# Performance work log

Hardware: AMD Instinct MI355X
Metric: run time of the kernel (lower is better)

The kernel has to match this reference:

```python
import jax, jax.numpy as jnp
import numpy as np

NUM_AA, EMB_DIM = 20, 16
H1, H2 = 128, 128
K, EXCLUDE = 64, 3
R_ON, R_CUT = 10.0, 12.0
RBF_CENTERS = (5.0, 6.0, 7.0, 8.0, 9.0, 10.0, 11.0)
RBF_WIDTH = 0.5
M = len(RBF_CENTERS)


def setup_inputs() -> dict:
    key = jax.random.key(0)
    ks = jax.random.split(key, 10)
    B, L = 8, 2048
    R = jax.random.normal(ks[0], (B, L, 3), dtype=jnp.float32) * 10.0  # spread distances over RBF range
    seq = jax.random.randint(ks[1], (B, L), 0, NUM_AA)
    emb_table = jax.random.normal(ks[2], (NUM_AA, EMB_DIM), dtype=jnp.float32) * 0.1
    in_dim = 3 * EMB_DIM
    W1 = jax.random.normal(ks[3], (in_dim, H1), dtype=jnp.float32) / np.sqrt(in_dim)
    b1 = jnp.zeros((H1,), jnp.float32)
    W2 = jax.random.normal(ks[4], (H1, H2), dtype=jnp.float32) / np.sqrt(H1)
    b2 = jnp.zeros((H2,), jnp.float32)
    W3 = jax.random.normal(ks[5], (H2, M), dtype=jnp.float32) / np.sqrt(H2)
    b3 = jnp.zeros((M,), jnp.float32)
    centers = jnp.asarray(RBF_CENTERS, jnp.float32)
    widths = jnp.full((M,), RBF_WIDTH, jnp.float32)
    return {"R": R, "seq": seq, "emb_table": emb_table,
            "W1": W1, "b1": b1, "W2": W2, "b2": b2, "W3": W3, "b3": b3,
            "centers": centers, "widths": widths}


def topk_nonbonded_pairs(R, K, exclude):
    # R: (B, L, 3) -> r: (B, L, K) distances, j: (B, L, K) neighbor indices
    B, L, _ = R.shape
    diff = R[:, :, None, :] - R[:, None, :, :]            # (B, L, L, 3)
    D = jnp.sqrt(jnp.sum(diff * diff, axis=-1) + 1e-12)   # (B, L, L)
    idx = jnp.arange(L)
    bonded = jnp.abs(idx[:, None] - idx[None, :]) <= exclude  # excludes self too
    D = jnp.where(bonded[None], jnp.inf, D)
    neg, j = jax.lax.top_k(-D, K)                          # K smallest distances
    return -neg, j


def smooth_switch(r, r_on, r_cut):
    t = jnp.clip((r - r_on) / (r_cut - r_on), 0.0, 1.0)
    return 1.0 - t * t * (3.0 - 2.0 * t)  # smoothstep down: 1 below r_on, 0 above r_cut


def distance_features(r, centers, widths):
    d = r[..., None] - centers  # (B, L, K, M)
    return jnp.exp(-(d * d) / (2.0 * widths * widths))


def reference(R, seq, emb_table, W1, b1, W2, b2, W3, b3, centers, widths):
    e = emb_table[seq]                                     # (B, L, d)
    r, j = topk_nonbonded_pairs(R, K, EXCLUDE)             # (B, L, K)
    e_j = jnp.take_along_axis(e[:, :, None, :], j[..., None], axis=1)  # wrong axis semantics avoided below
    # gather neighbor embeddings: e_j[b, i, k] = e[b, j[b, i, k]]
    e_j = jnp.take_along_axis(e[:, None, :, :].repeat(1, axis=1), j[..., None], axis=2) if False else \
          jnp.take_along_axis(e[:, :, None, :].transpose(0, 2, 1, 3).repeat(1, axis=0), j[..., None], axis=2) if False else \
          jax.vmap(lambda eb, jb: eb[jb])(e, j)            # (B, L, K, d)
    e_i = jnp.broadcast_to(e[:, :, None, :], e_j.shape)
    pair_feat = jnp.concatenate([e_i, e_j, e_i * e_j], axis=-1)  # (B, L, K, 3d)
    h = jax.nn.relu(pair_feat @ W1 + b1)
    h = jax.nn.relu(h @ W2 + b2)
    w = jax.nn.softplus(h @ W3 + b3)                       # (B, L, K, M)
    phi = distance_features(r, centers, widths)            # (B, L, K, M)
    att = -jnp.sum(w * phi, axis=-1)                       # (B, L, K)
    sw = smooth_switch(r, R_ON, R_CUT)
    return jnp.sum(att * sw, axis=(1, 2))                  # (B,)
```

## Files before the change

kernel.cpp:

```cpp
#include <hip/hip_runtime.h>
#include <math.h>

#define LSEQ 2048
#define KNB 64
#define BATCH 8
#define MRBF 7
#define NTILES 8192
#define NBLOCKS 512
#define BSCALE (255.0f/144.0f)

typedef __attribute__((ext_vector_type(8))) short short8;
typedef __attribute__((ext_vector_type(4))) float floatx4;

__device__ __forceinline__ unsigned short f2bf(float f) {
    unsigned u = __float_as_uint(f);
    u += 0x7fffu + ((u >> 16) & 1u);
    return (unsigned short)(u >> 16);
}
__device__ __forceinline__ unsigned pkbf(float a, float b) {
    return __builtin_amdgcn_perm(__float_as_uint(b) + 0x8000u,
                                 __float_as_uint(a) + 0x8000u, 0x07060302u);
}

__global__ __launch_bounds__(256, 2) void fused_kernel(
    const float* __restrict__ R, const int* __restrict__ seq,
    const float* __restrict__ emb,
    const float* __restrict__ W1, const float* __restrict__ b1,
    const float* __restrict__ W2, const float* __restrict__ b2,
    const float* __restrict__ W3, const float* __restrict__ b3,
    const float* __restrict__ centers, const float* __restrict__ widths,
    float* __restrict__ out)
{
    __shared__ __align__(16) unsigned short lds[32768];
    unsigned short* H1s = lds;
    unsigned short* Xs  = lds + 16384;
    unsigned short* H2s = lds + 16384;
    int*      nbrL    = (int*)lds;
    unsigned* hist    = (unsigned*)((char*)lds + 512);
    float*    cand_d2 = (float*)((char*)lds + 2560);
    int*      cand_j  = (int*)((char*)lds + 3584);
    int*      tctr    = (int*)((char*)lds + 4608);
    int* sB    = tctr + 0;
    int* sNeed = tctr + 2;
    int* oPos  = tctr + 4;
    int* cCnt  = tctr + 6;
    int* fCnt  = tctr + 8;
    __shared__ float bacc[BATCH];

    const int tid  = threadIdx.x;
    const int lane = tid & 63;
    const int wv   = tid >> 6;
    const int l15  = lane & 15;
    const int q    = lane >> 4;

    short8 w1f[2][2], w2f[2][4], w3f[4];
    float b1v[2][4], b2v[2][4];
    #pragma unroll
    for (int mtl = 0; mtl < 2; mtl++) {
        int m = (2*wv + mtl)*16 + l15;
        #pragma unroll
        for (int d = 0; d < 4; d++) {
            b1v[mtl][d] = b1[(2*wv + mtl)*16 + q*4 + d];
            b2v[mtl][d] = b2[(2*wv + mtl)*16 + q*4 + d];
        }
        #pragma unroll
        for (int kt = 0; kt < 2; kt++)
            #pragma unroll
            for (int jj = 0; jj < 8; jj++) {
                int k = kt*32 + q*8 + jj;
                w1f[mtl][kt][jj] = (short)((k < 48) ? f2bf(W1[k*128 + m]) : 0);
            }
        #pragma unroll
        for (int kt = 0; kt < 4; kt++)
            #pragma unroll
            for (int jj = 0; jj < 8; jj++) {
                int k = kt*32 + q*8 + jj;
                w2f[mtl][kt][jj] = (short)f2bf(W2[k*128 + m]);
            }
    }
    #pragma unroll
    for (int kt = 0; kt < 4; kt++)
        #pragma unroll
        for (int jj = 0; jj < 8; jj++) {
            int k = kt*32 + q*8 + jj;
            w3f[kt][jj] = (short)((l15 < MRBF) ? f2bf(W3[k*MRBF + l15]) : 0);
        }
    float b3C[4], cen[4], i2w[4];
    #pragma unroll
    for (int d = 0; d < 4; d++) {
        int rb = q*4 + d;
        bool ok = rb < MRBF;
        b3C[d] = ok ? b3[rb] : 0.f;
        cen[d] = ok ? centers[rb] : 0.f;
        float wd = ok ? widths[rb] : 1.f;
        i2w[d] = 0.5f / (wd*wd);
    }
    if (tid < BATCH) bacc[tid] = 0.f;

    const int pl = tid >> 1, half = tid & 1;
    const int s7p = pl & 7;
    float rloc = 0.f;

    for (int tile = blockIdx.x; tile < NTILES; tile += NBLOCKS) {
        const int b     = tile >> 10;
        const int ibase = (tile & 1023) << 1;
        const float* Rb = R + ((b << 11) * 3);

        __syncthreads();

        hist[tid] = 0u; hist[tid + 256] = 0u;
        if (tid < 2) { oPos[tid] = 0; cCnt[tid] = 0; fCnt[tid] = 0; }

        float px[8], py[8], pz[8];
        {
            const float4* rp = (const float4*)(Rb + tid*24);
            float4 f0=rp[0], f1=rp[1], f2=rp[2], f3=rp[3], f4=rp[4], f5=rp[5];
            px[0]=f0.x; py[0]=f0.y; pz[0]=f0.z;
            px[1]=f0.w; py[1]=f1.x; pz[1]=f1.y;
            px[2]=f1.z; py[2]=f1.w; pz[2]=f2.x;
            px[3]=f2.y; py[3]=f2.z; pz[3]=f2.w;
            px[4]=f3.x; py[4]=f3.y; pz[4]=f3.z;
            px[5]=f3.w; py[5]=f4.x; pz[5]=f4.y;
            px[6]=f4.z; py[6]=f4.w; pz[6]=f5.x;
            px[7]=f5.y; py[7]=f5.z; pz[7]=f5.w;
        }
        float cx0 = Rb[3*ibase+0], cy0 = Rb[3*ibase+1], cz0 = Rb[3*ibase+2];
        float cx1 = Rb[3*ibase+3], cy1 = Rb[3*ibase+4], cz1 = Rb[3*ibase+5];
        __syncthreads();

        float d2r[2][8];
        #pragma unroll
        for (int u = 0; u < 8; u++) {
            int j = tid*8 + u;
            #pragma unroll
            for (int c = 0; c < 2; c++) {
                float dx = (c ? cx1 : cx0) - px[u];
                float dy = (c ? cy1 : cy0) - py[u];
                float dz = (c ? cz1 : cz0) - pz[u];
                float d2 = dx*dx + dy*dy + dz*dz;
                int dd = j - (ibase + c); dd = dd < 0 ? -dd : dd;
                if (dd <= 3) d2 = 1e30f;
                d2r[c][u] = d2;
                if (d2 < 144.0f)
                    atomicAdd(&hist[(c<<8) + (int)(d2*BSCALE)], 1u);
            }
        }
        __syncthreads();

        if (wv < 2) {
            unsigned h4[4]; unsigned s = 0;
            #pragma unroll
            for (int v = 0; v < 4; v++) { h4[v] = hist[(wv<<8) + lane*4 + v]; s += h4[v]; }
            unsigned inc = s;
            #pragma unroll
            for (int off = 1; off < 64; off <<= 1) {
                unsigned n = __shfl_up(inc, off, 64);
                if (lane >= off) inc += n;
            }
            unsigned tot = __shfl(inc, 63, 64);
            unsigned excl = inc - s;
            if (tot < 64u) {
                if (lane == 0) { sB[wv] = 255; sNeed[wv] = 64 - (int)tot; }
            } else if (excl < 64u && 64u <= inc) {
                unsigned cc = excl;
                #pragma unroll
                for (int v = 0; v < 4; v++) {
                    if (cc < 64u && 64u <= cc + h4[v]) { sB[wv] = lane*4+v; sNeed[wv] = 64 - (int)cc; }
                    cc += h4[v];
                }
            }
        }
        __syncthreads();

        #pragma unroll
        for (int u = 0; u < 8; u++) {
            int j = tid*8 + u;
            #pragma unroll
            for (int c = 0; c < 2; c++) {
                float d2 = d2r[c][u];
                int B = sB[c];
                if (d2 < 144.0f) {
                    int key = (int)(d2*BSCALE);
                    if (key < B) {
                        int pos = atomicAdd(&oPos[c], 1);
                        nbrL[(c<<6) + pos] = j;
                    } else if (key == B) {
                        int cc = atomicAdd(&cCnt[c], 1);
                        if (cc < 128) { cand_d2[(c<<7)+cc] = d2; cand_j[(c<<7)+cc] = j; }
                    }
                } else if (B == 255 && d2 < 1e29f) {
                    int t = atomicAdd(&fCnt[c], 1);
                    if (t < sNeed[c]) {
                        int pos = atomicAdd(&oPos[c], 1);
                        nbrL[(c<<6) + pos] = j;
                    }
                }
            }
        }
        __syncthreads();

        if (wv < 2) {
            int B = sB[wv];
            if (B != 255) {
                int cn = cCnt[wv]; if (cn > 128) cn = 128;
                int need = sNeed[wv];
                for (int ci = lane; ci < cn; ci += 64) {
                    float dv = cand_d2[(wv<<7)+ci]; int jv = cand_j[(wv<<7)+ci];
                    int rank = 0;
                    for (int x = 0; x < cn; x++) {
                        float dx2 = cand_d2[(wv<<7)+x]; int jx2 = cand_j[(wv<<7)+x];
                        rank += (dx2 < dv) || (dx2 == dv && jx2 < jv);
                    }
                    if (rank < need) {
                        int pos = atomicAdd(&oPos[wv], 1);
                        nbrL[(wv<<6) + pos] = jv;
                    }
                }
            }
        }
        __syncthreads();

        {
            int c  = pl >> 6;
            int bi = (b << 11) + ibase + c;
            int j  = nbrL[pl];
            int rowj = (b << 11) + j;
            int si = seq[bi], sj = seq[rowj];
            const float4* ei = (const float4*)(emb + si*16 + half*8);
            const float4* ej = (const float4*)(emb + sj*16 + half*8);
            float4 eA0 = ei[0], eA1 = ei[1], eB0 = ej[0], eB1 = ej[1];
            int rb = pl*64;
            uint4 vA = make_uint4(pkbf(eA0.x,eA0.y), pkbf(eA0.z,eA0.w),
                                  pkbf(eA1.x,eA1.y), pkbf(eA1.z,eA1.w));
            uint4 vB = make_uint4(pkbf(eB0.x,eB0.y), pkbf(eB0.z,eB0.w),
                                  pkbf(eB1.x,eB1.y), pkbf(eB1.z,eB1.w));
            uint4 vP = make_uint4(pkbf(eA0.x*eB0.x, eA0.y*eB0.y),
                                  pkbf(eA0.z*eB0.z, eA0.w*eB0.w),
                                  pkbf(eA1.x*eB1.x, eA1.y*eB1.y),
                                  pkbf(eA1.z*eB1.z, eA1.w*eB1.w));
            *(uint4*)&Xs[rb + (((0|half)^s7p)<<3)] = vA;
            *(uint4*)&Xs[rb + (((2|half)^s7p)<<3)] = vB;
            *(uint4*)&Xs[rb + (((4|half)^s7p)<<3)] = vP;
            *(uint4*)&Xs[rb + (((6|half)^s7p)<<3)] = make_uint4(0u,0u,0u,0u);
            if (!half) {
                float dx = R[bi*3+0]-R[rowj*3+0];
                float dy = R[bi*3+1]-R[rowj*3+1];
                float dz = R[bi*3+2]-R[rowj*3+2];
                rloc = sqrtf(dx*dx + dy*dy + dz*dz + 1e-12f);
            }
        }
        __syncthreads();

        #pragma unroll
        for (int nt = 0; nt < 8; nt++) {
            int row = nt*16 + l15;
            int s7 = l15 & 7;
            const unsigned short* xr = Xs + row*64;
            short8 x0 = *(const short8*)&xr[(( q    ^ s7) << 3)];
            short8 x1 = *(const short8*)&xr[(((4|q) ^ s7) << 3)];
            #pragma unroll
            for (int mtl = 0; mtl < 2; mtl++) {
                floatx4 acc = {b1v[mtl][0], b1v[mtl][1], b1v[mtl][2], b1v[mtl][3]};
                acc = __builtin_amdgcn_mfma_f32_16x16x32_bf16(w1f[mtl][0], x0, acc, 0, 0, 0);
                acc = __builtin_amdgcn_mfma_f32_16x16x32_bf16(w1f[mtl][1], x1, acc, 0, 0, 0);
                int chnk = (((2*wv + mtl)*2 + (q>>1)) ^ s7);
                *(uint2*)&H1s[row*128 + (chnk<<3) + ((q&1)<<2)] =
                    make_uint2(pkbf(fmaxf(acc[0],0.f), fmaxf(acc[1],0.f)),
                               pkbf(fmaxf(acc[2],0.f), fmaxf(acc[3],0.f)));
            }
        }
        __syncthreads();

        #pragma unroll
        for (int nt = 0; nt < 8; nt++) {
            int row = nt*16 + l15;
            int s7 = l15 & 7;
            const unsigned short* hr = H1s + row*128;
            short8 hf0 = *(const short8*)&hr[(( q     ^ s7) << 3)];
            short8 hf1 = *(const short8*)&hr[((( 4|q) ^ s7) << 3)];
            short8 hf2 = *(const short8*)&hr[((( 8|q) ^ s7) << 3)];
            short8 hf3 = *(const short8*)&hr[(((12|q) ^ s7) << 3)];
            #pragma unroll
            for (int mtl = 0; mtl < 2; mtl++) {
                floatx4 acc = {b2v[mtl][0], b2v[mtl][1], b2v[mtl][2], b2v[mtl][3]};
                acc = __builtin_amdgcn_mfma_f32_16x16x32_bf16(w2f[mtl][0], hf0, acc, 0, 0, 0);
                acc = __builtin_amdgcn_mfma_f32_16x16x32_bf16(w2f[mtl][1], hf1, acc, 0, 0, 0);
                acc = __builtin_amdgcn_mfma_f32_16x16x32_bf16(w2f[mtl][2], hf2, acc, 0, 0, 0);
                acc = __builtin_amdgcn_mfma_f32_16x16x32_bf16(w2f[mtl][3], hf3, acc, 0, 0, 0);
                int chnk = (((2*wv + mtl)*2 + (q>>1)) ^ s7);
                *(uint2*)&H2s[row*128 + (chnk<<3) + ((q&1)<<2)] =
                    make_uint2(pkbf(fmaxf(acc[0],0.f), fmaxf(acc[1],0.f)),
                               pkbf(fmaxf(acc[2],0.f), fmaxf(acc[3],0.f)));
            }
        }
        __syncthreads();

        float esum = 0.f;
        #pragma unroll
        for (int ntl = 0; ntl < 2; ntl++) {
            int nt = 2*wv + ntl;
            int row = nt*16 + l15;
            int s7 = l15 & 7;
            const unsigned short* hr = H2s + row*128;
            floatx4 a3 = {b3C[0], b3C[1], b3C[2], b3C[3]};
            #pragma unroll
            for (int kt = 0; kt < 4; kt++) {
                short8 hf = *(const short8*)&hr[((((kt<<2)|q) ^ s7) << 3)];
                a3 = __builtin_amdgcn_mfma_f32_16x16x32_bf16(w3f[kt], hf, a3, 0, 0, 0);
            }
            float rr = __shfl(rloc, (ntl<<5) + 2*l15, 64);
            if (rr < 12.0f) {
                float att = 0.f;
                #pragma unroll
                for (int d = 0; d < 4; d++) {
                    if (q*4 + d < MRBF) {
                        float x = a3[d];
                        float sp = fmaxf(x, 0.f) + __logf(1.f + __expf(-fabsf(x)));
                        float df = rr - cen[d];
                        att += sp * __expf(-df*df*i2w[d]);
                    }
                }
                att += __shfl_xor(att, 16, 64);
                att += __shfl_xor(att, 32, 64);
                float t = fminf(fmaxf((rr - 10.f)*0.5f, 0.f), 1.f);
                float sw = 1.f - t*t*(3.f - 2.f*t);
                esum -= att * sw;
            }
        }
        #pragma unroll
        for (int off = 1; off < 64; off <<= 1)
            esum += __shfl_xor(esum, off, 64);
        if (lane == 0) atomicAdd(&bacc[b], esum * 0.25f);
    }
    __syncthreads();
    if (tid < BATCH) atomicAdd(&out[tid], bacc[tid]);
}

extern "C" void kernel_launch(void* const* d_in, const int* in_sizes, int n_in,
                              void* d_out, int out_size, void* d_ws, size_t ws_size,
                              hipStream_t stream) {
    const float* R       = (const float*)d_in[0];
    const int*   seq     = (const int*)  d_in[1];
    const float* emb     = (const float*)d_in[2];
    const float* W1      = (const float*)d_in[3];
    const float* b1      = (const float*)d_in[4];
    const float* W2      = (const float*)d_in[5];
    const float* b2      = (const float*)d_in[6];
    const float* W3      = (const float*)d_in[7];
    const float* b3      = (const float*)d_in[8];
    const float* centers = (const float*)d_in[9];
    const float* widths  = (const float*)d_in[10];
    float* out = (float*)d_out;

    hipMemsetAsync(d_out, 0, out_size * sizeof(float), stream);

    fused_kernel<<<NBLOCKS, 256, 0, stream>>>(R, seq, emb, W1, b1, W2, b2, W3, b3,
                                              centers, widths, out);
}
```

Baseline: 253.7 us.

## Process four query rows per block iteration and shrink LDS for three blocks per CU

```diff
diff --git a/kernel.cpp b/kernel.cpp
--- a/kernel.cpp
+++ b/kernel.cpp
@@ -5,8 +5,8 @@
 #define KNB 64
 #define BATCH 8
 #define MRBF 7
-#define NTILES 8192
-#define NBLOCKS 512
+#define NGROUPS 4096
+#define NBLOCKS 768
 #define BSCALE (255.0f/144.0f)
 
 typedef __attribute__((ext_vector_type(8))) short short8;
@@ -22,7 +22,7 @@
                                  __float_as_uint(a) + 0x8000u, 0x07060302u);
 }
 
-__global__ __launch_bounds__(256, 2) void fused_kernel(
+__global__ __launch_bounds__(256, 3) void fused_kernel(
     const float* __restrict__ R, const int* __restrict__ seq,
     const float* __restrict__ emb,
     const float* __restrict__ W1, const float* __restrict__ b1,
@@ -31,20 +31,19 @@
     const float* __restrict__ centers, const float* __restrict__ widths,
     float* __restrict__ out)
 {
-    __shared__ __align__(16) unsigned short lds[32768];
-    unsigned short* H1s = lds;
-    unsigned short* Xs  = lds + 16384;
-    unsigned short* H2s = lds + 16384;
-    int*      nbrL    = (int*)lds;
-    unsigned* hist    = (unsigned*)((char*)lds + 512);
-    float*    cand_d2 = (float*)((char*)lds + 2560);
-    int*      cand_j  = (int*)((char*)lds + 3584);
-    int*      tctr    = (int*)((char*)lds + 4608);
+    __shared__ __align__(16) unsigned short lds[25088];
+    int* nbrL = (int*)lds;
+    unsigned short* Xs = lds + 512;
+    unsigned short* Hs = lds + 8704;
+    unsigned* hist    = (unsigned*)((char*)lds + 1024);
+    float*    cand_d2 = (float*)((char*)lds + 5120);
+    int*      cand_j  = (int*)((char*)lds + 7168);
+    int*      tctr    = (int*)((char*)lds + 9216);
     int* sB    = tctr + 0;
-    int* sNeed = tctr + 2;
-    int* oPos  = tctr + 4;
-    int* cCnt  = tctr + 6;
-    int* fCnt  = tctr + 8;
+    int* sNeed = tctr + 4;
+    int* oPos  = tctr + 8;
+    int* cCnt  = tctr + 12;
+    int* fCnt  = tctr + 16;
     __shared__ float bacc[BATCH];
 
     const int tid  = threadIdx.x;
@@ -101,15 +100,13 @@
     const int s7p = pl & 7;
     float rloc = 0.f;
 
-    for (int tile = blockIdx.x; tile < NTILES; tile += NBLOCKS) {
-        const int b     = tile >> 10;
-        const int ibase = (tile & 1023) << 1;
+    for (int grp = blockIdx.x; grp < NGROUPS; grp += NBLOCKS) {
+        const int b     = grp >> 9;
+        const int ibase = (grp & 511) << 2;
         const float* Rb = R + ((b << 11) * 3);
 
-        __syncthreads();
-
-        hist[tid] = 0u; hist[tid + 256] = 0u;
-        if (tid < 2) { oPos[tid] = 0; cCnt[tid] = 0; fCnt[tid] = 0; }
+        hist[tid] = 0u; hist[tid+256] = 0u; hist[tid+512] = 0u; hist[tid+768] = 0u;
+        if (tid < 4) { oPos[tid] = 0; cCnt[tid] = 0; fCnt[tid] = 0; }
 
         float px[8], py[8], pz[8];
         {
@@ -124,19 +121,22 @@
             px[6]=f4.z; py[6]=f4.w; pz[6]=f5.x;
             px[7]=f5.y; py[7]=f5.z; pz[7]=f5.w;
         }
-        float cx0 = Rb[3*ibase+0], cy0 = Rb[3*ibase+1], cz0 = Rb[3*ibase+2];
-        float cx1 = Rb[3*ibase+3], cy1 = Rb[3*ibase+4], cz1 = Rb[3*ibase+5];
-        __syncthreads();
-
-        float d2r[2][8];
+        float cx[4], cy[4], cz[4];
+        #pragma unroll
+        for (int c = 0; c < 4; c++) {
+            cx[c] = Rb[3*(ibase+c)+0];
+            cy[c] = Rb[3*(ibase+c)+1];
+            cz[c] = Rb[3*(ibase+c)+2];
+        }
+        __syncthreads();
+
+        float d2r[4][8];
         #pragma unroll
         for (int u = 0; u < 8; u++) {
             int j = tid*8 + u;
             #pragma unroll
-            for (int c = 0; c < 2; c++) {
-                float dx = (c ? cx1 : cx0) - px[u];
-                float dy = (c ? cy1 : cy0) - py[u];
-                float dz = (c ? cz1 : cz0) - pz[u];
+            for (int c = 0; c < 4; c++) {
+                float dx = cx[c]-px[u], dy = cy[c]-py[u], dz = cz[c]-pz[u];
                 float d2 = dx*dx + dy*dy + dz*dz;
                 int dd = j - (ibase + c); dd = dd < 0 ? -dd : dd;
                 if (dd <= 3) d2 = 1e30f;
@@ -147,7 +147,7 @@
         }
         __syncthreads();
 
-        if (wv < 2) {
+        {
             unsigned h4[4]; unsigned s = 0;
             #pragma unroll
             for (int v = 0; v < 4; v++) { h4[v] = hist[(wv<<8) + lane*4 + v]; s += h4[v]; }
@@ -176,7 +176,7 @@
         for (int u = 0; u < 8; u++) {
             int j = tid*8 + u;
             #pragma unroll
-            for (int c = 0; c < 2; c++) {
+            for (int c = 0; c < 4; c++) {
                 float d2 = d2r[c][u];
                 int B = sB[c];
                 if (d2 < 144.0f) {
@@ -199,7 +199,7 @@
         }
         __syncthreads();
 
-        if (wv < 2) {
+        {
             int B = sB[wv];
             if (B != 255) {
                 int cn = cCnt[wv]; if (cn > 128) cn = 128;
@@ -220,111 +220,124 @@
         }
         __syncthreads();
 
-        {
-            int c  = pl >> 6;
-            int bi = (b << 11) + ibase + c;
-            int j  = nbrL[pl];
-            int rowj = (b << 11) + j;
-            int si = seq[bi], sj = seq[rowj];
-            const float4* ei = (const float4*)(emb + si*16 + half*8);
-            const float4* ej = (const float4*)(emb + sj*16 + half*8);
-            float4 eA0 = ei[0], eA1 = ei[1], eB0 = ej[0], eB1 = ej[1];
-            int rb = pl*64;
-            uint4 vA = make_uint4(pkbf(eA0.x,eA0.y), pkbf(eA0.z,eA0.w),
-                                  pkbf(eA1.x,eA1.y), pkbf(eA1.z,eA1.w));
-            uint4 vB = make_uint4(pkbf(eB0.x,eB0.y), pkbf(eB0.z,eB0.w),
-                                  pkbf(eB1.x,eB1.y), pkbf(eB1.z,eB1.w));
-            uint4 vP = make_uint4(pkbf(eA0.x*eB0.x, eA0.y*eB0.y),
-                                  pkbf(eA0.z*eB0.z, eA0.w*eB0.w),
-                                  pkbf(eA1.x*eB1.x, eA1.y*eB1.y),
-                                  pkbf(eA1.z*eB1.z, eA1.w*eB1.w));
-            *(uint4*)&Xs[rb + (((0|half)^s7p)<<3)] = vA;
-            *(uint4*)&Xs[rb + (((2|half)^s7p)<<3)] = vB;
-            *(uint4*)&Xs[rb + (((4|half)^s7p)<<3)] = vP;
-            *(uint4*)&Xs[rb + (((6|half)^s7p)<<3)] = make_uint4(0u,0u,0u,0u);
-            if (!half) {
-                float dx = R[bi*3+0]-R[rowj*3+0];
-                float dy = R[bi*3+1]-R[rowj*3+1];
-                float dz = R[bi*3+2]-R[rowj*3+2];
-                rloc = sqrtf(dx*dx + dy*dy + dz*dz + 1e-12f);
-            }
-        }
-        __syncthreads();
-
-        #pragma unroll
-        for (int nt = 0; nt < 8; nt++) {
-            int row = nt*16 + l15;
-            int s7 = l15 & 7;
-            const unsigned short* xr = Xs + row*64;
-            short8 x0 = *(const short8*)&xr[(( q    ^ s7) << 3)];
-            short8 x1 = *(const short8*)&xr[(((4|q) ^ s7) << 3)];
-            #pragma unroll
-            for (int mtl = 0; mtl < 2; mtl++) {
-                floatx4 acc = {b1v[mtl][0], b1v[mtl][1], b1v[mtl][2], b1v[mtl][3]};
-                acc = __builtin_amdgcn_mfma_f32_16x16x32_bf16(w1f[mtl][0], x0, acc, 0, 0, 0);
-                acc = __builtin_amdgcn_mfma_f32_16x16x32_bf16(w1f[mtl][1], x1, acc, 0, 0, 0);
-                int chnk = (((2*wv + mtl)*2 + (q>>1)) ^ s7);
-                *(uint2*)&H1s[row*128 + (chnk<<3) + ((q&1)<<2)] =
-                    make_uint2(pkbf(fmaxf(acc[0],0.f), fmaxf(acc[1],0.f)),
-                               pkbf(fmaxf(acc[2],0.f), fmaxf(acc[3],0.f)));
-            }
-        }
-        __syncthreads();
-
-        #pragma unroll
-        for (int nt = 0; nt < 8; nt++) {
-            int row = nt*16 + l15;
-            int s7 = l15 & 7;
-            const unsigned short* hr = H1s + row*128;
-            short8 hf0 = *(const short8*)&hr[(( q     ^ s7) << 3)];
-            short8 hf1 = *(const short8*)&hr[((( 4|q) ^ s7) << 3)];
-            short8 hf2 = *(const short8*)&hr[((( 8|q) ^ s7) << 3)];
-            short8 hf3 = *(const short8*)&hr[(((12|q) ^ s7) << 3)];
-            #pragma unroll
-            for (int mtl = 0; mtl < 2; mtl++) {
-                floatx4 acc = {b2v[mtl][0], b2v[mtl][1], b2v[mtl][2], b2v[mtl][3]};
-                acc = __builtin_amdgcn_mfma_f32_16x16x32_bf16(w2f[mtl][0], hf0, acc, 0, 0, 0);
-                acc = __builtin_amdgcn_mfma_f32_16x16x32_bf16(w2f[mtl][1], hf1, acc, 0, 0, 0);
-                acc = __builtin_amdgcn_mfma_f32_16x16x32_bf16(w2f[mtl][2], hf2, acc, 0, 0, 0);
-                acc = __builtin_amdgcn_mfma_f32_16x16x32_bf16(w2f[mtl][3], hf3, acc, 0, 0, 0);
-                int chnk = (((2*wv + mtl)*2 + (q>>1)) ^ s7);
-                *(uint2*)&H2s[row*128 + (chnk<<3) + ((q&1)<<2)] =
-                    make_uint2(pkbf(fmaxf(acc[0],0.f), fmaxf(acc[1],0.f)),
-                               pkbf(fmaxf(acc[2],0.f), fmaxf(acc[3],0.f)));
-            }
-        }
-        __syncthreads();
-
         float esum = 0.f;
-        #pragma unroll
-        for (int ntl = 0; ntl < 2; ntl++) {
-            int nt = 2*wv + ntl;
-            int row = nt*16 + l15;
-            int s7 = l15 & 7;
-            const unsigned short* hr = H2s + row*128;
-            floatx4 a3 = {b3C[0], b3C[1], b3C[2], b3C[3]};
-            #pragma unroll
-            for (int kt = 0; kt < 4; kt++) {
-                short8 hf = *(const short8*)&hr[((((kt<<2)|q) ^ s7) << 3)];
-                a3 = __builtin_amdgcn_mfma_f32_16x16x32_bf16(w3f[kt], hf, a3, 0, 0, 0);
-            }
-            float rr = __shfl(rloc, (ntl<<5) + 2*l15, 64);
-            if (rr < 12.0f) {
-                float att = 0.f;
-                #pragma unroll
-                for (int d = 0; d < 4; d++) {
-                    if (q*4 + d < MRBF) {
-                        float x = a3[d];
-                        float sp = fmaxf(x, 0.f) + __logf(1.f + __expf(-fabsf(x)));
-                        float df = rr - cen[d];
-                        att += sp * __expf(-df*df*i2w[d]);
-                    }
-                }
-                att += __shfl_xor(att, 16, 64);
-                att += __shfl_xor(att, 32, 64);
-                float t = fminf(fmaxf((rr - 10.f)*0.5f, 0.f), 1.f);
-                float sw = 1.f - t*t*(3.f - 2.f*t);
-                esum -= att * sw;
+        #pragma unroll 1
+        for (int sub = 0; sub < 2; sub++) {
+            {
+                int c2 = (sub << 1) | (pl >> 6);
+                int bi = (b << 11) + ibase + c2;
+                int j  = nbrL[(c2 << 6) + (pl & 63)];
+                int rowj = (b << 11) + j;
+                int si = seq[bi], sj = seq[rowj];
+                const float4* ei = (const float4*)(emb + si*16 + half*8);
+                const float4* ej = (const float4*)(emb + sj*16 + half*8);
+                float4 eA0 = ei[0], eA1 = ei[1], eB0 = ej[0], eB1 = ej[1];
+                int rb = pl*64;
+                uint4 vA = make_uint4(pkbf(eA0.x,eA0.y), pkbf(eA0.z,eA0.w),
+                                      pkbf(eA1.x,eA1.y), pkbf(eA1.z,eA1.w));
+                uint4 vB = make_uint4(pkbf(eB0.x,eB0.y), pkbf(eB0.z,eB0.w),
+                                      pkbf(eB1.x,eB1.y), pkbf(eB1.z,eB1.w));
+                uint4 vP = make_uint4(pkbf(eA0.x*eB0.x, eA0.y*eB0.y),
+                                      pkbf(eA0.z*eB0.z, eA0.w*eB0.w),
+                                      pkbf(eA1.x*eB1.x, eA1.y*eB1.y),
+                                      pkbf(eA1.z*eB1.z, eA1.w*eB1.w));
+                *(uint4*)&Xs[rb + (((0|half)^s7p)<<3)] = vA;
+                *(uint4*)&Xs[rb + (((2|half)^s7p)<<3)] = vB;
+                *(uint4*)&Xs[rb + (((4|half)^s7p)<<3)] = vP;
+                *(uint4*)&Xs[rb + (((6|half)^s7p)<<3)] = make_uint4(0u,0u,0u,0u);
+                if (!half) {
+                    float dx = R[bi*3+0]-R[rowj*3+0];
+                    float dy = R[bi*3+1]-R[rowj*3+1];
+                    float dz = R[bi*3+2]-R[rowj*3+2];
+                    rloc = sqrtf(dx*dx + dy*dy + dz*dz + 1e-12f);
+                }
+            }
+            __syncthreads();
+
+            #pragma unroll
+            for (int nt = 0; nt < 8; nt++) {
+                int row = nt*16 + l15;
+                int s7 = l15 & 7;
+                const unsigned short* xr = Xs + row*64;
+                short8 x0 = *(const short8*)&xr[(( q    ^ s7) << 3)];
+                short8 x1 = *(const short8*)&xr[(((4|q) ^ s7) << 3)];
+                #pragma unroll
+                for (int mtl = 0; mtl < 2; mtl++) {
+                    floatx4 acc = {b1v[mtl][0], b1v[mtl][1], b1v[mtl][2], b1v[mtl][3]};
+                    acc = __builtin_amdgcn_mfma_f32_16x16x32_bf16(w1f[mtl][0], x0, acc, 0, 0, 0);
+                    acc = __builtin_amdgcn_mfma_f32_16x16x32_bf16(w1f[mtl][1], x1, acc, 0, 0, 0);
+                    int chnk = (((2*wv + mtl)*2 + (q>>1)) ^ s7);
+                    *(uint2*)&Hs[row*128 + (chnk<<3) + ((q&1)<<2)] =
+                        make_uint2(pkbf(fmaxf(acc[0],0.f), fmaxf(acc[1],0.f)),
+                                   pkbf(fmaxf(acc[2],0.f), fmaxf(acc[3],0.f)));
+                }
+            }
+            __syncthreads();
+
+            uint2 h2p[8][2];
+            #pragma unroll
+            for (int nt = 0; nt < 8; nt++) {
+                int row = nt*16 + l15;
+                int s7 = l15 & 7;
+                const unsigned short* hr = Hs + row*128;
+                short8 hf0 = *(const short8*)&hr[(( q     ^ s7) << 3)];
+                short8 hf1 = *(const short8*)&hr[((( 4|q) ^ s7) << 3)];
+                short8 hf2 = *(const short8*)&hr[((( 8|q) ^ s7) << 3)];
+                short8 hf3 = *(const short8*)&hr[(((12|q) ^ s7) << 3)];
+                #pragma unroll
+                for (int mtl = 0; mtl < 2; mtl++) {
+                    floatx4 acc = {b2v[mtl][0], b2v[mtl][1], b2v[mtl][2], b2v[mtl][3]};
+                    acc = __builtin_amdgcn_mfma_f32_16x16x32_bf16(w2f[mtl][0], hf0, acc, 0, 0, 0);
+                    acc = __builtin_amdgcn_mfma_f32_16x16x32_bf16(w2f[mtl][1], hf1, acc, 0, 0, 0);
+                    acc = __builtin_amdgcn_mfma_f32_16x16x32_bf16(w2f[mtl][2], hf2, acc, 0, 0, 0);
+                    acc = __builtin_amdgcn_mfma_f32_16x16x32_bf16(w2f[mtl][3], hf3, acc, 0, 0, 0);
+                    h2p[nt][mtl] = make_uint2(pkbf(fmaxf(acc[0],0.f), fmaxf(acc[1],0.f)),
+                                              pkbf(fmaxf(acc[2],0.f), fmaxf(acc[3],0.f)));
+                }
+            }
+            __syncthreads();
+            #pragma unroll
+            for (int nt = 0; nt < 8; nt++) {
+                int row = nt*16 + l15;
+                int s7 = l15 & 7;
+                #pragma unroll
+                for (int mtl = 0; mtl < 2; mtl++) {
+                    int chnk = (((2*wv + mtl)*2 + (q>>1)) ^ s7);
+                    *(uint2*)&Hs[row*128 + (chnk<<3) + ((q&1)<<2)] = h2p[nt][mtl];
+                }
+            }
+            __syncthreads();
+
+            #pragma unroll
+            for (int ntl = 0; ntl < 2; ntl++) {
+                int nt = 2*wv + ntl;
+                int row = nt*16 + l15;
+                int s7 = l15 & 7;
+                const unsigned short* hr = Hs + row*128;
+                floatx4 a3 = {b3C[0], b3C[1], b3C[2], b3C[3]};
+                #pragma unroll
+                for (int kt = 0; kt < 4; kt++) {
+                    short8 hf = *(const short8*)&hr[((((kt<<2)|q) ^ s7) << 3)];
+                    a3 = __builtin_amdgcn_mfma_f32_16x16x32_bf16(w3f[kt], hf, a3, 0, 0, 0);
+                }
+                float rr = __shfl(rloc, (ntl<<5) + 2*l15, 64);
+                if (rr < 12.0f) {
+                    float att = 0.f;
+                    #pragma unroll
+                    for (int d = 0; d < 4; d++) {
+                        if (q*4 + d < MRBF) {
+                            float x = a3[d];
+                            float sp = fmaxf(x, 0.f) + __logf(1.f + __expf(-fabsf(x)));
+                            float df = rr - cen[d];
+                            att += sp * __expf(-df*df*i2w[d]);
+                        }
+                    }
+                    att += __shfl_xor(att, 16, 64);
+                    att += __shfl_xor(att, 32, 64);
+                    float t = fminf(fmaxf((rr - 10.f)*0.5f, 0.f), 1.f);
+                    float sw = 1.f - t*t*(3.f - 2.f*t);
+                    esum -= att * sw;
+                }
             }
         }
         #pragma unroll
```

New measurement: 371.4 us. 46.4% more time.

## Double block to 512 threads, one MFMA tile per wave, reuse one hidden buffer

Applied to the files above, without the earlier changes.

```diff
diff --git a/kernel.cpp b/kernel.cpp
--- a/kernel.cpp
+++ b/kernel.cpp
@@ -22,7 +22,7 @@
                                  __float_as_uint(a) + 0x8000u, 0x07060302u);
 }
 
-__global__ __launch_bounds__(256, 2) void fused_kernel(
+__global__ __launch_bounds__(512, 4) void fused_kernel(
     const float* __restrict__ R, const int* __restrict__ seq,
     const float* __restrict__ emb,
     const float* __restrict__ W1, const float* __restrict__ b1,
@@ -31,20 +31,14 @@
     const float* __restrict__ centers, const float* __restrict__ widths,
     float* __restrict__ out)
 {
-    __shared__ __align__(16) unsigned short lds[32768];
-    unsigned short* H1s = lds;
-    unsigned short* Xs  = lds + 16384;
-    unsigned short* H2s = lds + 16384;
-    int*      nbrL    = (int*)lds;
-    unsigned* hist    = (unsigned*)((char*)lds + 512);
-    float*    cand_d2 = (float*)((char*)lds + 2560);
-    int*      cand_j  = (int*)((char*)lds + 3584);
-    int*      tctr    = (int*)((char*)lds + 4608);
-    int* sB    = tctr + 0;
-    int* sNeed = tctr + 2;
-    int* oPos  = tctr + 4;
-    int* cCnt  = tctr + 6;
-    int* fCnt  = tctr + 8;
+    __shared__ __align__(16) unsigned short lds[24576];
+    unsigned short* Xs = lds;
+    unsigned short* Hs = lds + 8192;
+    float* cand_d2 = (float*)lds;
+    int*   cand_j  = (int*)(lds + 512);
+    __shared__ int      nbrL[128];
+    __shared__ unsigned hist[512];
+    __shared__ int sB[2], sNeed[2], oPos[2], cCnt[2], fCnt[2];
     __shared__ float bacc[BATCH];
 
     const int tid  = threadIdx.x;
@@ -53,38 +47,37 @@
     const int l15  = lane & 15;
     const int q    = lane >> 4;
 
-    short8 w1f[2][2], w2f[2][4], w3f[4];
-    float b1v[2][4], b2v[2][4];
-    #pragma unroll
-    for (int mtl = 0; mtl < 2; mtl++) {
-        int m = (2*wv + mtl)*16 + l15;
+    short8 w1f[2], w2f[4], w3f[4];
+    float b1v[4], b2v[4];
+    {
+        int m = wv*16 + l15;
         #pragma unroll
         for (int d = 0; d < 4; d++) {
-            b1v[mtl][d] = b1[(2*wv + mtl)*16 + q*4 + d];
-            b2v[mtl][d] = b2[(2*wv + mtl)*16 + q*4 + d];
+            b1v[d] = b1[wv*16 + q*4 + d];
+            b2v[d] = b2[wv*16 + q*4 + d];
         }
         #pragma unroll
         for (int kt = 0; kt < 2; kt++)
             #pragma unroll
             for (int jj = 0; jj < 8; jj++) {
                 int k = kt*32 + q*8 + jj;
-                w1f[mtl][kt][jj] = (short)((k < 48) ? f2bf(W1[k*128 + m]) : 0);
+                w1f[kt][jj] = (short)((k < 48) ? f2bf(W1[k*128 + m]) : 0);
             }
         #pragma unroll
         for (int kt = 0; kt < 4; kt++)
             #pragma unroll
             for (int jj = 0; jj < 8; jj++) {
                 int k = kt*32 + q*8 + jj;
-                w2f[mtl][kt][jj] = (short)f2bf(W2[k*128 + m]);
+                w2f[kt][jj] = (short)f2bf(W2[k*128 + m]);
+            }
+        #pragma unroll
+        for (int kt = 0; kt < 4; kt++)
+            #pragma unroll
+            for (int jj = 0; jj < 8; jj++) {
+                int k = kt*32 + q*8 + jj;
+                w3f[kt][jj] = (short)((l15 < MRBF) ? f2bf(W3[k*MRBF + l15]) : 0);
             }
     }
-    #pragma unroll
-    for (int kt = 0; kt < 4; kt++)
-        #pragma unroll
-        for (int jj = 0; jj < 8; jj++) {
-            int k = kt*32 + q*8 + jj;
-            w3f[kt][jj] = (short)((l15 < MRBF) ? f2bf(W3[k*MRBF + l15]) : 0);
-        }
     float b3C[4], cen[4], i2w[4];
     #pragma unroll
     for (int d = 0; d < 4; d++) {
@@ -97,7 +90,7 @@
     }
     if (tid < BATCH) bacc[tid] = 0.f;
 
-    const int pl = tid >> 1, half = tid & 1;
+    const int pl = tid >> 2, qd = tid & 3;
     const int s7p = pl & 7;
     float rloc = 0.f;
 
@@ -106,32 +99,26 @@
         const int ibase = (tile & 1023) << 1;
         const float* Rb = R + ((b << 11) * 3);
 
-        __syncthreads();
-
-        hist[tid] = 0u; hist[tid + 256] = 0u;
+        hist[tid & 511] = 0u;
         if (tid < 2) { oPos[tid] = 0; cCnt[tid] = 0; fCnt[tid] = 0; }
 
-        float px[8], py[8], pz[8];
+        float px[4], py[4], pz[4];
         {
-            const float4* rp = (const float4*)(Rb + tid*24);
-            float4 f0=rp[0], f1=rp[1], f2=rp[2], f3=rp[3], f4=rp[4], f5=rp[5];
+            const float4* rp = (const float4*)(Rb + tid*12);
+            float4 f0 = rp[0], f1 = rp[1], f2 = rp[2];
             px[0]=f0.x; py[0]=f0.y; pz[0]=f0.z;
             px[1]=f0.w; py[1]=f1.x; pz[1]=f1.y;
             px[2]=f1.z; py[2]=f1.w; pz[2]=f2.x;
             px[3]=f2.y; py[3]=f2.z; pz[3]=f2.w;
-            px[4]=f3.x; py[4]=f3.y; pz[4]=f3.z;
-            px[5]=f3.w; py[5]=f4.x; pz[5]=f4.y;
-            px[6]=f4.z; py[6]=f4.w; pz[6]=f5.x;
-            px[7]=f5.y; py[7]=f5.z; pz[7]=f5.w;
         }
         float cx0 = Rb[3*ibase+0], cy0 = Rb[3*ibase+1], cz0 = Rb[3*ibase+2];
         float cx1 = Rb[3*ibase+3], cy1 = Rb[3*ibase+4], cz1 = Rb[3*ibase+5];
         __syncthreads();
 
-        float d2r[2][8];
-        #pragma unroll
-        for (int u = 0; u < 8; u++) {
-            int j = tid*8 + u;
+        float d2r[2][4];
+        #pragma unroll
+        for (int u = 0; u < 4; u++) {
+            int j = tid*4 + u;
             #pragma unroll
             for (int c = 0; c < 2; c++) {
                 float dx = (c ? cx1 : cx0) - px[u];
@@ -173,8 +160,8 @@
         __syncthreads();
 
         #pragma unroll
-        for (int u = 0; u < 8; u++) {
-            int j = tid*8 + u;
+        for (int u = 0; u < 4; u++) {
+            int j = tid*4 + u;
             #pragma unroll
             for (int c = 0; c < 2; c++) {
                 float d2 = d2r[c][u];
@@ -226,23 +213,26 @@
             int j  = nbrL[pl];
             int rowj = (b << 11) + j;
             int si = seq[bi], sj = seq[rowj];
-            const float4* ei = (const float4*)(emb + si*16 + half*8);
-            const float4* ej = (const float4*)(emb + sj*16 + half*8);
-            float4 eA0 = ei[0], eA1 = ei[1], eB0 = ej[0], eB1 = ej[1];
+            const float* ep = emb + ((qd < 2) ? si : sj)*16 + (qd & 1)*8;
+            float4 ea0 = *(const float4*)ep;
+            float4 ea1 = *(const float4*)(ep + 4);
+            float4 pb0, pb1;
+            pb0.x = __shfl_xor(ea0.x, 2, 64); pb0.y = __shfl_xor(ea0.y, 2, 64);
+            pb0.z = __shfl_xor(ea0.z, 2, 64); pb0.w = __shfl_xor(ea0.w, 2, 64);
+            pb1.x = __shfl_xor(ea1.x, 2, 64); pb1.y = __shfl_xor(ea1.y, 2, 64);
+            pb1.z = __shfl_xor(ea1.z, 2, 64); pb1.w = __shfl_xor(ea1.w, 2, 64);
             int rb = pl*64;
-            uint4 vA = make_uint4(pkbf(eA0.x,eA0.y), pkbf(eA0.z,eA0.w),
-                                  pkbf(eA1.x,eA1.y), pkbf(eA1.z,eA1.w));
-            uint4 vB = make_uint4(pkbf(eB0.x,eB0.y), pkbf(eB0.z,eB0.w),
-                                  pkbf(eB1.x,eB1.y), pkbf(eB1.z,eB1.w));
-            uint4 vP = make_uint4(pkbf(eA0.x*eB0.x, eA0.y*eB0.y),
-                                  pkbf(eA0.z*eB0.z, eA0.w*eB0.w),
-                                  pkbf(eA1.x*eB1.x, eA1.y*eB1.y),
-                                  pkbf(eA1.z*eB1.z, eA1.w*eB1.w));
-            *(uint4*)&Xs[rb + (((0|half)^s7p)<<3)] = vA;
-            *(uint4*)&Xs[rb + (((2|half)^s7p)<<3)] = vB;
-            *(uint4*)&Xs[rb + (((4|half)^s7p)<<3)] = vP;
-            *(uint4*)&Xs[rb + (((6|half)^s7p)<<3)] = make_uint4(0u,0u,0u,0u);
-            if (!half) {
+            uint4 v0 = make_uint4(pkbf(ea0.x,ea0.y), pkbf(ea0.z,ea0.w),
+                                  pkbf(ea1.x,ea1.y), pkbf(ea1.z,ea1.w));
+            uint4 v1 = (qd < 2)
+                ? make_uint4(pkbf(ea0.x*pb0.x, ea0.y*pb0.y),
+                             pkbf(ea0.z*pb0.z, ea0.w*pb0.w),
+                             pkbf(ea1.x*pb1.x, ea1.y*pb1.y),
+                             pkbf(ea1.z*pb1.z, ea1.w*pb1.w))
+                : make_uint4(0u, 0u, 0u, 0u);
+            *(uint4*)&Xs[rb + ((qd       ^ s7p) << 3)] = v0;
+            *(uint4*)&Xs[rb + (((qd + 4) ^ s7p) << 3)] = v1;
+            if (qd == 0) {
                 float dx = R[bi*3+0]-R[rowj*3+0];
                 float dy = R[bi*3+1]-R[rowj*3+1];
                 float dz = R[bi*3+2]-R[rowj*3+2];
@@ -258,57 +248,56 @@
             const unsigned short* xr = Xs + row*64;
             short8 x0 = *(const short8*)&xr[(( q    ^ s7) << 3)];
             short8 x1 = *(const short8*)&xr[(((4|q) ^ s7) << 3)];
-            #pragma unroll
-            for (int mtl = 0; mtl < 2; mtl++) {
-                floatx4 acc = {b1v[mtl][0], b1v[mtl][1], b1v[mtl][2], b1v[mtl][3]};
-                acc = __builtin_amdgcn_mfma_f32_16x16x32_bf16(w1f[mtl][0], x0, acc, 0, 0, 0);
-                acc = __builtin_amdgcn_mfma_f32_16x16x32_bf16(w1f[mtl][1], x1, acc, 0, 0, 0);
-                int chnk = (((2*wv + mtl)*2 + (q>>1)) ^ s7);
-                *(uint2*)&H1s[row*128 + (chnk<<3) + ((q&1)<<2)] =
-                    make_uint2(pkbf(fmaxf(acc[0],0.f), fmaxf(acc[1],0.f)),
-                               pkbf(fmaxf(acc[2],0.f), fmaxf(acc[3],0.f)));
-            }
-        }
-        __syncthreads();
-
+            floatx4 acc = {b1v[0], b1v[1], b1v[2], b1v[3]};
+            acc = __builtin_amdgcn_mfma_f32_16x16x32_bf16(w1f[0], x0, acc, 0, 0, 0);
+            acc = __builtin_amdgcn_mfma_f32_16x16x32_bf16(w1f[1], x1, acc, 0, 0, 0);
+            int chnk = ((wv*2 + (q>>1)) ^ s7);
+            *(uint2*)&Hs[row*128 + (chnk<<3) + ((q&1)<<2)] =
+                make_uint2(pkbf(fmaxf(acc[0],0.f), fmaxf(acc[1],0.f)),
+                           pkbf(fmaxf(acc[2],0.f), fmaxf(acc[3],0.f)));
+        }
+        __syncthreads();
+
+        uint2 h2p[8];
         #pragma unroll
         for (int nt = 0; nt < 8; nt++) {
             int row = nt*16 + l15;
             int s7 = l15 & 7;
-            const unsigned short* hr = H1s + row*128;
+            const unsigned short* hr = Hs + row*128;
             short8 hf0 = *(const short8*)&hr[(( q     ^ s7) << 3)];
             short8 hf1 = *(const short8*)&hr[((( 4|q) ^ s7) << 3)];
             short8 hf2 = *(const short8*)&hr[((( 8|q) ^ s7) << 3)];
             short8 hf3 = *(const short8*)&hr[(((12|q) ^ s7) << 3)];
-            #pragma unroll
-            for (int mtl = 0; mtl < 2; mtl++) {
-                floatx4 acc = {b2v[mtl][0], b2v[mtl][1], b2v[mtl][2], b2v[mtl][3]};
-                acc = __builtin_amdgcn_mfma_f32_16x16x32_bf16(w2f[mtl][0], hf0, acc, 0, 0, 0);
-                acc = __builtin_amdgcn_mfma_f32_16x16x32_bf16(w2f[mtl][1], hf1, acc, 0, 0, 0);
-                acc = __builtin_amdgcn_mfma_f32_16x16x32_bf16(w2f[mtl][2], hf2, acc, 0, 0, 0);
-                acc = __builtin_amdgcn_mfma_f32_16x16x32_bf16(w2f[mtl][3], hf3, acc, 0, 0, 0);
-                int chnk = (((2*wv + mtl)*2 + (q>>1)) ^ s7);
-                *(uint2*)&H2s[row*128 + (chnk<<3) + ((q&1)<<2)] =
-                    make_uint2(pkbf(fmaxf(acc[0],0.f), fmaxf(acc[1],0.f)),
-                               pkbf(fmaxf(acc[2],0.f), fmaxf(acc[3],0.f)));
-            }
-        }
-        __syncthreads();
-
-        float esum = 0.f;
-        #pragma unroll
-        for (int ntl = 0; ntl < 2; ntl++) {
-            int nt = 2*wv + ntl;
+            floatx4 acc = {b2v[0], b2v[1], b2v[2], b2v[3]};
+            acc = __builtin_amdgcn_mfma_f32_16x16x32_bf16(w2f[0], hf0, acc, 0, 0, 0);
+            acc = __builtin_amdgcn_mfma_f32_16x16x32_bf16(w2f[1], hf1, acc, 0, 0, 0);
+            acc = __builtin_amdgcn_mfma_f32_16x16x32_bf16(w2f[2], hf2, acc, 0, 0, 0);
+            acc = __builtin_amdgcn_mfma_f32_16x16x32_bf16(w2f[3], hf3, acc, 0, 0, 0);
+            h2p[nt] = make_uint2(pkbf(fmaxf(acc[0],0.f), fmaxf(acc[1],0.f)),
+                                 pkbf(fmaxf(acc[2],0.f), fmaxf(acc[3],0.f)));
+        }
+        __syncthreads();
+        #pragma unroll
+        for (int nt = 0; nt < 8; nt++) {
             int row = nt*16 + l15;
             int s7 = l15 & 7;
-            const unsigned short* hr = H2s + row*128;
+            int chnk = ((wv*2 + (q>>1)) ^ s7);
+            *(uint2*)&Hs[row*128 + (chnk<<3) + ((q&1)<<2)] = h2p[nt];
+        }
+        __syncthreads();
+
+        float esum = 0.f;
+        {
+            int row = wv*16 + l15;
+            int s7 = l15 & 7;
+            const unsigned short* hr = Hs + row*128;
             floatx4 a3 = {b3C[0], b3C[1], b3C[2], b3C[3]};
             #pragma unroll
             for (int kt = 0; kt < 4; kt++) {
                 short8 hf = *(const short8*)&hr[((((kt<<2)|q) ^ s7) << 3)];
                 a3 = __builtin_amdgcn_mfma_f32_16x16x32_bf16(w3f[kt], hf, a3, 0, 0, 0);
             }
-            float rr = __shfl(rloc, (ntl<<5) + 2*l15, 64);
+            float rr = __shfl(rloc, 4*l15, 64);
             if (rr < 12.0f) {
                 float att = 0.f;
                 #pragma unroll
@@ -354,6 +343,6 @@
 
     hipMemsetAsync(d_out, 0, out_size * sizeof(float), stream);
 
-    fused_kernel<<<NBLOCKS, 256, 0, stream>>>(R, seq, emb, W1, b1, W2, b2, W3, b3,
+    fused_kernel<<<NBLOCKS, 512, 0, stream>>>(R, seq, emb, W1, b1, W2, b2, W3, b3,
                                               centers, widths, out);
 }
```

After: 258.8 us. No clear change (+2.0%).
